# Kernel optimization log

Hardware: AMD Instinct MI355X
Metric: run time of the kernel (lower is better)

Reference implementation:

```python
import jax, jax.numpy as jnp
import numpy as np
from jax import lax

D_MODEL = 1024
D_STATE = 16
D_CONV = 4
EXPAND = 2
D_INNER = D_MODEL * EXPAND
EPS = 1e-6


def setup_inputs() -> dict:
    key = jax.random.key(0)
    ks = jax.random.split(key, 8)
    B, L = 2, 1024
    x = jax.random.normal(ks[0], (B, L, D_MODEL), dtype=jnp.float32)
    norm_w = jnp.ones((D_MODEL,), jnp.float32)
    W_in = jax.random.normal(ks[1], (2 * D_INNER, D_MODEL), jnp.float32) * (1.0 / np.sqrt(D_MODEL))
    conv_w = jax.random.normal(ks[2], (D_INNER, 1, D_CONV), jnp.float32) * (1.0 / np.sqrt(D_CONV))
    conv_b = jnp.zeros((D_INNER,), jnp.float32)
    W_x = jax.random.normal(ks[3], (2 * D_STATE + 1, D_INNER), jnp.float32) * (1.0 / np.sqrt(D_INNER))
    A_log = jnp.log(jnp.broadcast_to(jnp.arange(1, D_STATE + 1, dtype=jnp.float32), (D_INNER, D_STATE)))
    D_skip = jnp.ones((D_INNER,), jnp.float32)
    W_dt = jax.random.normal(ks[4], (D_INNER, 1), jnp.float32)
    b_dt = jax.random.normal(ks[5], (D_INNER,), jnp.float32) * 0.1
    W_out = jax.random.normal(ks[6], (D_MODEL, D_INNER), jnp.float32) * (1.0 / np.sqrt(D_INNER))
    return {"x": x, "norm_w": norm_w, "W_in": W_in, "conv_w": conv_w, "conv_b": conv_b,
            "W_x": W_x, "A_log": A_log, "D_skip": D_skip, "W_dt": W_dt, "b_dt": b_dt, "W_out": W_out}


def _selective_scan(x, delta, A, Bp, Cp, D_skip):
    # x, delta: (B, L, D); A: (D, N); Bp, Cp: (B, L, N)
    Bb, L, Dd = x.shape
    N = A.shape[1]

    def step(h, t_in):
        delta_t, B_t, C_t, x_t = t_in           # (B,D),(B,N),(B,N),(B,D)
        dA = jnp.exp(delta_t[..., None] * A)    # (B,D,N)
        h = dA * h + (delta_t * x_t)[..., None] * B_t[:, None, :]
        y_t = jnp.einsum('bdn,bn->bd', h, C_t)
        return h, y_t

    xs = (jnp.moveaxis(delta, 1, 0), jnp.moveaxis(Bp, 1, 0),
          jnp.moveaxis(Cp, 1, 0), jnp.moveaxis(x, 1, 0))
    h0 = jnp.zeros((Bb, Dd, N), x.dtype)
    _, ys = lax.scan(step, h0, xs)              # ys: (L,B,D)
    return jnp.moveaxis(ys, 0, 1) + x * D_skip


def reference(x, norm_w, W_in, conv_w, conv_b, W_x, A_log, D_skip, W_dt, b_dt, W_out):
    residual = x
    # RMSNorm
    xn = x * lax.rsqrt(jnp.mean(x * x, axis=-1, keepdims=True) + EPS) * norm_w
    # in_proj and split
    xz = xn @ W_in.T                              # (B,L,2*Din)
    x_ssm, z = jnp.split(xz, 2, axis=-1)
    # causal depthwise conv1d
    xc = jnp.swapaxes(x_ssm, 1, 2)                # (B,Din,L)
    xc = lax.conv_general_dilated(xc, conv_w, window_strides=(1,),
                                  padding=[(D_CONV - 1, 0)],
                                  feature_group_count=D_INNER,
                                  dimension_numbers=('NCH', 'OIH', 'NCH'))
    xc = xc + conv_b[None, :, None]
    x_ssm = jax.nn.silu(jnp.swapaxes(xc, 1, 2))   # (B,L,Din)
    # input-dependent SSM params
    ssm_params = x_ssm @ W_x.T                    # (B,L,2N+1)
    B_param = ssm_params[:, :, :D_STATE]
    C_param = ssm_params[:, :, D_STATE:2 * D_STATE]
    dt_raw = ssm_params[:, :, -1:]                # (B,L,1)
    delta = jax.nn.softplus(dt_raw * W_dt[:, 0] + b_dt)  # (B,L,Din)
    A = -jnp.exp(A_log)
    y = _selective_scan(x_ssm, delta, A, B_param, C_param, D_skip)
    y = y * jax.nn.silu(z)
    y = y @ W_out.T
    return y + residual
```

## Files before the change

kernel.cpp:

```cpp
#include <hip/hip_runtime.h>
#include <math.h>

#define D_MODEL 1024
#define D_STATE 16
#define D_CONV  4
#define D_INNER 2048
#define LSEQ    1024
#define BATCH   2
#define NROWS   (BATCH * LSEQ)
#define EPSV    1e-6f

#define CHUNK   64
#define NCHUNK  (LSEQ / CHUNK)
#define SSTATE  (BATCH * D_INNER * D_STATE)
#define SROW    36

typedef __attribute__((ext_vector_type(8))) short bf16x8;
typedef __attribute__((ext_vector_type(4))) float f32x4;

__device__ __forceinline__ float silu_f(float x) { return x / (1.0f + __expf(-x)); }
__device__ __forceinline__ float softplus_f(float x) {
    return (x > 20.0f) ? x : __logf(1.0f + __expf(x));
}
__device__ __forceinline__ unsigned short f2bf(float f) {
    unsigned int u = __float_as_uint(f);
    unsigned int r = (u + 0x7FFFu + ((u >> 16) & 1u)) >> 16;
    return (unsigned short)r;
}

__global__ __launch_bounds__(256) void cvt_bf16_kernel(const float* __restrict__ src,
                                                       unsigned short* __restrict__ dst) {
    int i = blockIdx.x * 256 + threadIdx.x;
    float4 v = ((const float4*)src)[i];
    ushort4 o;
    o.x = f2bf(v.x); o.y = f2bf(v.y); o.z = f2bf(v.z); o.w = f2bf(v.w);
    ((ushort4*)dst)[i] = o;
}

__global__ __launch_bounds__(256) void rmsnorm_kernel(const float* __restrict__ x,
                                                      const float* __restrict__ w,
                                                      unsigned short* __restrict__ xnb) {
    int row = blockIdx.x;
    const float4* xr = (const float4*)(x + (size_t)row * D_MODEL);
    float4 v = xr[threadIdx.x];
    float s = v.x * v.x + v.y * v.y + v.z * v.z + v.w * v.w;
#pragma unroll
    for (int off = 32; off > 0; off >>= 1) s += __shfl_down(s, off, 64);
    __shared__ float wsum[4];
    int lane = threadIdx.x & 63, wv = threadIdx.x >> 6;
    if (lane == 0) wsum[wv] = s;
    __syncthreads();
    float tot = wsum[0] + wsum[1] + wsum[2] + wsum[3];
    float scale = rsqrtf(tot * (1.0f / D_MODEL) + EPSV);
    const float4* wr = (const float4*)w;
    float4 wv4 = wr[threadIdx.x];
    ushort4 o;
    o.x = f2bf(v.x * scale * wv4.x);
    o.y = f2bf(v.y * scale * wv4.y);
    o.z = f2bf(v.z * scale * wv4.z);
    o.w = f2bf(v.w * scale * wv4.w);
    ((ushort4*)(xnb + (size_t)row * D_MODEL))[threadIdx.x] = o;
}

template<int TM, int TN, int JL>
__global__ __launch_bounds__(256) void gemm_bt_db(const short* __restrict__ A,
                                                  const short* __restrict__ B,
                                                  float* __restrict__ C,
                                                  const float* __restrict__ resid,
                                                  int M, int N, int K) {
    constexpr int MI = TM / 32, NJ = TN / 32;
    __shared__ alignas(16) short As[2][TM * 32];
    __shared__ alignas(16) short Bs[2][TN * 32];
    int tid = threadIdx.x;
    int wave = tid >> 6, lane = tid & 63;
    int wm = (wave >> 1) * (TM / 2), wn = (wave & 1) * (TN / 2);
    int m0 = blockIdx.y * TM, n0 = blockIdx.x * TN;

    f32x4 acc[MI][NJ];
#pragma unroll
    for (int i = 0; i < MI; i++)
#pragma unroll
        for (int j = 0; j < NJ; j++) acc[i][j] = (f32x4){0.f, 0.f, 0.f, 0.f};

    const short* Ab = A + (size_t)m0 * K;
    const short* Bb = B + (size_t)n0 * K;
    int qk = (lane >> 4) * 8;
    int rr = lane & 15;

    auto stage = [&](int k0, int buf) {
#pragma unroll
        for (int c0 = 0; c0 < TM * 4; c0 += 256) {
            int c = c0 + tid;
            __builtin_amdgcn_global_load_lds(
                (const __attribute__((address_space(1))) void*)(Ab + (size_t)(c >> 2) * K + k0 + (c & 3) * 8),
                (__attribute__((address_space(3))) void*)(&As[buf][c * 8]), 16, 0, 0);
        }
#pragma unroll
        for (int c0 = 0; c0 < TN * 4; c0 += 256) {
            int c = c0 + tid;
            __builtin_amdgcn_global_load_lds(
                (const __attribute__((address_space(1))) void*)(Bb + (size_t)(c >> 2) * K + k0 + (c & 3) * 8),
                (__attribute__((address_space(3))) void*)(&Bs[buf][c * 8]), 16, 0, 0);
        }
    };

    stage(0, 0);
    int KI = K / 32;
    for (int ki = 0; ki < KI; ki++) {
        int b = ki & 1;
        if (ki + 1 < KI) {
            stage((ki + 1) * 32, b ^ 1);
            __builtin_amdgcn_s_waitcnt(0xF70 | JL);
        } else {
            __builtin_amdgcn_s_waitcnt(0xF70);
        }
        __builtin_amdgcn_s_barrier();

        bf16x8 af[MI], bfr[NJ];
#pragma unroll
        for (int i = 0; i < MI; i++)
            af[i] = *(const bf16x8*)(&As[b][(wm + i * 16 + rr) * 32 + qk]);
#pragma unroll
        for (int j = 0; j < NJ; j++)
            bfr[j] = *(const bf16x8*)(&Bs[b][(wn + j * 16 + rr) * 32 + qk]);
#pragma unroll
        for (int i = 0; i < MI; i++)
#pragma unroll
            for (int j = 0; j < NJ; j++)
                acc[i][j] = __builtin_amdgcn_mfma_f32_16x16x32_bf16(af[i], bfr[j], acc[i][j], 0, 0, 0);
        __builtin_amdgcn_s_barrier();
    }

    int q4 = (lane >> 4) * 4;
#pragma unroll
    for (int i = 0; i < MI; i++) {
#pragma unroll
        for (int j = 0; j < NJ; j++) {
            int n = n0 + wn + j * 16 + rr;
#pragma unroll
            for (int v = 0; v < 4; v++) {
                int mm = m0 + wm + i * 16 + q4 + v;
                float val = acc[i][j][v];
                if (resid) val += resid[(size_t)mm * N + n];
                C[(size_t)mm * N + n] = val;
            }
        }
    }
}

__global__ __launch_bounds__(256) void conv_silu_kernel(const float* __restrict__ xz,
                                                        const float* __restrict__ w,
                                                        const float* __restrict__ cb,
                                                        float* __restrict__ xc) {
    int idx = blockIdx.x * 256 + threadIdx.x;
    int d = idx & (D_INNER - 1);
    int bl = idx >> 11;
    int l = bl & (LSEQ - 1);
    int bb = bl >> 10;
    float w0 = w[d * 4 + 0], w1 = w[d * 4 + 1], w2 = w[d * 4 + 2], w3 = w[d * 4 + 3];
    const float* base = xz + (size_t)(bb * LSEQ) * (2 * D_INNER) + d;
    float acc = cb[d];
    if (l >= 3) acc += w0 * base[(size_t)(l - 3) * (2 * D_INNER)];
    if (l >= 2) acc += w1 * base[(size_t)(l - 2) * (2 * D_INNER)];
    if (l >= 1) acc += w2 * base[(size_t)(l - 1) * (2 * D_INNER)];
    acc += w3 * base[(size_t)l * (2 * D_INNER)];
    xc[idx] = silu_f(acc);
}

#define PR 4
__global__ __launch_bounds__(256) void params_kernel(const float* __restrict__ xc,
                                                     const float* __restrict__ Wx,
                                                     float* __restrict__ ssm) {
    int r0 = blockIdx.x * PR;
    __shared__ alignas(16) float xs[PR][D_INNER];
    const float4* src = (const float4*)(xc + (size_t)r0 * D_INNER);
    for (int i = threadIdx.x; i < PR * D_INNER / 4; i += 256)
        ((float4*)xs)[i] = src[i];
    __syncthreads();
    int lane = threadIdx.x & 63, wv = threadIdx.x >> 6;
    for (int n = wv; n < 2 * D_STATE + 1; n += 4) {
        const float4* wrow = (const float4*)(Wx + (size_t)n * D_INNER);
        float s0 = 0.f, s1 = 0.f, s2 = 0.f, s3 = 0.f;
#pragma unroll
        for (int c = 0; c < D_INNER / 4 / 64; c++) {
            int k = c * 64 + lane;
            float4 w  = wrow[k];
            float4 a0 = *(const float4*)&xs[0][k * 4];
            float4 a1 = *(const float4*)&xs[1][k * 4];
            float4 a2 = *(const float4*)&xs[2][k * 4];
            float4 a3 = *(const float4*)&xs[3][k * 4];
            s0 += a0.x * w.x + a0.y * w.y + a0.z * w.z + a0.w * w.w;
            s1 += a1.x * w.x + a1.y * w.y + a1.z * w.z + a1.w * w.w;
            s2 += a2.x * w.x + a2.y * w.y + a2.z * w.z + a2.w * w.w;
            s3 += a3.x * w.x + a3.y * w.y + a3.z * w.z + a3.w * w.w;
        }
#pragma unroll
        for (int off = 32; off > 0; off >>= 1) {
            s0 += __shfl_down(s0, off, 64);
            s1 += __shfl_down(s1, off, 64);
            s2 += __shfl_down(s2, off, 64);
            s3 += __shfl_down(s3, off, 64);
        }
        if (lane == 0) {
            ssm[(size_t)(r0 + 0) * 33 + n] = s0;
            ssm[(size_t)(r0 + 1) * 33 + n] = s1;
            ssm[(size_t)(r0 + 2) * 33 + n] = s2;
            ssm[(size_t)(r0 + 3) * 33 + n] = s3;
        }
    }
}

__device__ __forceinline__ void stage_ssm(const float* __restrict__ ssm,
                                          float* __restrict__ s_ssm,
                                          int bb, int c, int tid) {
    int t = tid >> 2, j = tid & 3;
    const float* g = ssm + (size_t)(bb * LSEQ + c * CHUNK + t) * 33;
    float* s = s_ssm + t * SROW;
    for (int col = j; col < 33; col += 4) s[col] = g[col];
}

__global__ __launch_bounds__(256) void scanA_kernel(const float* __restrict__ ssm,
                                                    const float* __restrict__ xc,
                                                    const float* __restrict__ A_log,
                                                    const float* __restrict__ Wdt,
                                                    const float* __restrict__ bdt,
                                                    float* __restrict__ P,
                                                    float* __restrict__ Q) {
    int c = blockIdx.x, dg = blockIdx.y, bb = blockIdx.z;
    int tid = threadIdx.x;
    int d = dg * 256 + tid;
    __shared__ alignas(16) float s_ssm[CHUNK * SROW];
    stage_ssm(ssm, s_ssm, bb, c, tid);
    __syncthreads();

    float wdt = Wdt[d], bdtv = bdt[d];
    float Adn[16];
    {
        const float4* ar = (const float4*)(A_log + (size_t)d * 16);
#pragma unroll
        for (int r = 0; r < 4; r++) {
            float4 a = ar[r];
            Adn[r * 4 + 0] = -__expf(a.x);
            Adn[r * 4 + 1] = -__expf(a.y);
            Adn[r * 4 + 2] = -__expf(a.z);
            Adn[r * 4 + 3] = -__expf(a.w);
        }
    }
    float h[16];
#pragma unroll
    for (int n = 0; n < 16; n++) h[n] = 0.f;
    float sd = 0.f;
    const float* xg = xc + ((size_t)(bb * LSEQ + c * CHUNK)) * D_INNER + d;

#pragma unroll 2
    for (int t = 0; t < CHUNK; t++) {
        float dtr = s_ssm[t * SROW + 32];
        float dlt = softplus_f(dtr * wdt + bdtv);
        float xt = xg[(size_t)t * D_INNER];
        float u = dlt * xt;
        sd += dlt;
        const float4* Bq = (const float4*)&s_ssm[t * SROW];
#pragma unroll
        for (int r = 0; r < 4; r++) {
            float4 Bv = Bq[r];
            float dA0 = __expf(dlt * Adn[r * 4 + 0]);
            float dA1 = __expf(dlt * Adn[r * 4 + 1]);
            float dA2 = __expf(dlt * Adn[r * 4 + 2]);
            float dA3 = __expf(dlt * Adn[r * 4 + 3]);
            h[r * 4 + 0] = dA0 * h[r * 4 + 0] + u * Bv.x;
            h[r * 4 + 1] = dA1 * h[r * 4 + 1] + u * Bv.y;
            h[r * 4 + 2] = dA2 * h[r * 4 + 2] + u * Bv.z;
            h[r * 4 + 3] = dA3 * h[r * 4 + 3] + u * Bv.w;
        }
    }
    size_t idx = (size_t)c * SSTATE + ((size_t)bb * D_INNER + d) * 16;
#pragma unroll
    for (int r = 0; r < 4; r++) {
        float4 pv, qv;
        pv.x = __expf(Adn[r * 4 + 0] * sd);
        pv.y = __expf(Adn[r * 4 + 1] * sd);
        pv.z = __expf(Adn[r * 4 + 2] * sd);
        pv.w = __expf(Adn[r * 4 + 3] * sd);
        qv.x = h[r * 4 + 0]; qv.y = h[r * 4 + 1];
        qv.z = h[r * 4 + 2]; qv.w = h[r * 4 + 3];
        *(float4*)(P + idx + r * 4) = pv;
        *(float4*)(Q + idx + r * 4) = qv;
    }
}

__global__ __launch_bounds__(256) void scanB_kernel(float* __restrict__ P,
                                                    const float* __restrict__ Q) {
    int bdn = blockIdx.x * 256 + threadIdx.x;
    float H = 0.0f;
#pragma unroll
    for (int c = 0; c < NCHUNK; c++) {
        size_t idx = (size_t)c * SSTATE + bdn;
        float p = P[idx], q = Q[idx];
        P[idx] = H;
        H = p * H + q;
    }
}

__global__ __launch_bounds__(256) void scanC_kernel(const float* __restrict__ ssm,
                                                    const float* __restrict__ xc,
                                                    const float* __restrict__ xz,
                                                    const float* __restrict__ A_log,
                                                    const float* __restrict__ Wdt,
                                                    const float* __restrict__ bdt,
                                                    const float* __restrict__ Hs,
                                                    const float* __restrict__ Dskip,
                                                    unsigned short* __restrict__ yb) {
    int c = blockIdx.x, dg = blockIdx.y, bb = blockIdx.z;
    int tid = threadIdx.x;
    int d = dg * 256 + tid;
    __shared__ alignas(16) float s_ssm[CHUNK * SROW];
    stage_ssm(ssm, s_ssm, bb, c, tid);
    __syncthreads();

    float wdt = Wdt[d], bdtv = bdt[d], dsk = Dskip[d];
    float Adn[16];
    {
        const float4* ar = (const float4*)(A_log + (size_t)d * 16);
#pragma unroll
        for (int r = 0; r < 4; r++) {
            float4 a = ar[r];
            Adn[r * 4 + 0] = -__expf(a.x);
            Adn[r * 4 + 1] = -__expf(a.y);
            Adn[r * 4 + 2] = -__expf(a.z);
            Adn[r * 4 + 3] = -__expf(a.w);
        }
    }
    float h[16];
    {
        size_t idx = (size_t)c * SSTATE + ((size_t)bb * D_INNER + d) * 16;
#pragma unroll
        for (int r = 0; r < 4; r++) {
            float4 hv = *(const float4*)(Hs + idx + r * 4);
            h[r * 4 + 0] = hv.x; h[r * 4 + 1] = hv.y;
            h[r * 4 + 2] = hv.z; h[r * 4 + 3] = hv.w;
        }
    }
    const float* xg = xc + ((size_t)(bb * LSEQ + c * CHUNK)) * D_INNER + d;
    const float* zg = xz + ((size_t)(bb * LSEQ + c * CHUNK)) * (2 * D_INNER) + D_INNER + d;
    unsigned short* yg = yb + ((size_t)(bb * LSEQ + c * CHUNK)) * D_INNER + d;

#pragma unroll 2
    for (int t = 0; t < CHUNK; t++) {
        float dtr = s_ssm[t * SROW + 32];
        float dlt = softplus_f(dtr * wdt + bdtv);
        float xt = xg[(size_t)t * D_INNER];
        float zt = zg[(size_t)t * (2 * D_INNER)];
        float u = dlt * xt;
        const float4* Bq = (const float4*)&s_ssm[t * SROW];
        const float4* Cq = (const float4*)&s_ssm[t * SROW + 16];
        float y = 0.f;
#pragma unroll
        for (int r = 0; r < 4; r++) {
            float4 Bv = Bq[r];
            float4 Cv = Cq[r];
            float dA0 = __expf(dlt * Adn[r * 4 + 0]);
            float dA1 = __expf(dlt * Adn[r * 4 + 1]);
            float dA2 = __expf(dlt * Adn[r * 4 + 2]);
            float dA3 = __expf(dlt * Adn[r * 4 + 3]);
            h[r * 4 + 0] = dA0 * h[r * 4 + 0] + u * Bv.x;
            h[r * 4 + 1] = dA1 * h[r * 4 + 1] + u * Bv.y;
            h[r * 4 + 2] = dA2 * h[r * 4 + 2] + u * Bv.z;
            h[r * 4 + 3] = dA3 * h[r * 4 + 3] + u * Bv.w;
            y += h[r * 4 + 0] * Cv.x + h[r * 4 + 1] * Cv.y
               + h[r * 4 + 2] * Cv.z + h[r * 4 + 3] * Cv.w;
        }
        float o = (y + xt * dsk) * silu_f(zt);
        yg[(size_t)t * D_INNER] = f2bf(o);
    }
}

extern "C" void kernel_launch(void* const* d_in, const int* in_sizes, int n_in,
                              void* d_out, int out_size, void* d_ws, size_t ws_size,
                              hipStream_t stream) {
    const float* x      = (const float*)d_in[0];
    const float* norm_w = (const float*)d_in[1];
    const float* W_in   = (const float*)d_in[2];
    const float* conv_w = (const float*)d_in[3];
    const float* conv_b = (const float*)d_in[4];
    const float* W_x    = (const float*)d_in[5];
    const float* A_log  = (const float*)d_in[6];
    const float* D_skip = (const float*)d_in[7];
    const float* W_dt   = (const float*)d_in[8];
    const float* b_dt   = (const float*)d_in[9];
    const float* W_out  = (const float*)d_in[10];
    float* out = (float*)d_out;

    float* ws = (float*)d_ws;
    float* xz      = ws;
    float* xconv   = xz + (size_t)NROWS * 2 * D_INNER;
    float* ssm     = xconv + (size_t)NROWS * D_INNER;
    float* after   = ssm + (size_t)NROWS * 33;
    unsigned short* xnb    = (unsigned short*)after;
    unsigned short* W_in_b = (unsigned short*)(after + 1024 * 1024);
    unsigned short* W_out_b= (unsigned short*)(after + 3 * 1024 * 1024);
    unsigned short* ybuf_b = (unsigned short*)(after + 4 * 1024 * 1024);
    float* Pbuf = after + 1024 * 1024;
    float* Qbuf = Pbuf + (size_t)NCHUNK * SSTATE;

    cvt_bf16_kernel<<<(2 * D_INNER * D_MODEL) / 1024, 256, 0, stream>>>(W_in, W_in_b);
    cvt_bf16_kernel<<<(D_MODEL * D_INNER) / 1024, 256, 0, stream>>>(W_out, W_out_b);
    rmsnorm_kernel<<<NROWS, 256, 0, stream>>>(x, norm_w, xnb);
    {
        dim3 grid(2 * D_INNER / 128, NROWS / 64);
        gemm_bt_db<64, 128, 3><<<grid, 256, 0, stream>>>(
            (const short*)xnb, (const short*)W_in_b, xz, nullptr,
            NROWS, 2 * D_INNER, D_MODEL);
    }
    conv_silu_kernel<<<(NROWS * D_INNER) / 256, 256, 0, stream>>>(xz, conv_w, conv_b, xconv);
    params_kernel<<<NROWS / PR, 256, 0, stream>>>(xconv, W_x, ssm);
    {
        dim3 grid(NCHUNK, D_INNER / 256, BATCH);
        scanA_kernel<<<grid, 256, 0, stream>>>(ssm, xconv, A_log, W_dt, b_dt, Pbuf, Qbuf);
        scanB_kernel<<<SSTATE / 256, 256, 0, stream>>>(Pbuf, Qbuf);
        scanC_kernel<<<grid, 256, 0, stream>>>(ssm, xconv, xz, A_log, W_dt, b_dt,
                                               Pbuf, D_skip, ybuf_b);
    }
    {
        dim3 grid(D_MODEL / 64, NROWS / 64);
        gemm_bt_db<64, 64, 2><<<grid, 256, 0, stream>>>(
            (const short*)ybuf_b, (const short*)W_out_b, out, x,
            NROWS, D_MODEL, D_INNER);
    }
}
```

Measured before the change: 251.2 us.

## Split SSM state across 4 threads per channel in chunked scan kernels

The chunked scan kernels now give each channel to four threads, each holding four of the sixteen state entries, and reduce the C-projection with cross-lane shuffles. The grid grows fourfold along the channel axis. This shortens each thread's serial dependency chain and register footprint and raises the number of waves. In exchange, softplus, the x and z loads and the staging of shared memory are repeated across four times as many threads and blocks, and output stores are issued by only a quarter of the lanes.

```diff
diff --git a/kernel.cpp b/kernel.cpp
--- a/kernel.cpp
+++ b/kernel.cpp
@@ -210,6 +210,7 @@
     }
 }
 
+
 __device__ __forceinline__ void stage_ssm(const float* __restrict__ ssm,
                                           float* __restrict__ s_ssm,
                                           int bb, int c, int tid) {
@@ -228,64 +229,43 @@
                                                     float* __restrict__ Q) {
     int c = blockIdx.x, dg = blockIdx.y, bb = blockIdx.z;
     int tid = threadIdx.x;
-    int d = dg * 256 + tid;
+    int ch = tid >> 2, sg = tid & 3;
+    int d = dg * 64 + ch;
     __shared__ alignas(16) float s_ssm[CHUNK * SROW];
     stage_ssm(ssm, s_ssm, bb, c, tid);
     __syncthreads();
 
     float wdt = Wdt[d], bdtv = bdt[d];
-    float Adn[16];
-    {
-        const float4* ar = (const float4*)(A_log + (size_t)d * 16);
-#pragma unroll
-        for (int r = 0; r < 4; r++) {
-            float4 a = ar[r];
-            Adn[r * 4 + 0] = -__expf(a.x);
-            Adn[r * 4 + 1] = -__expf(a.y);
-            Adn[r * 4 + 2] = -__expf(a.z);
-            Adn[r * 4 + 3] = -__expf(a.w);
-        }
-    }
-    float h[16];
-#pragma unroll
-    for (int n = 0; n < 16; n++) h[n] = 0.f;
+    float Adn[4];
+    {
+        float4 a = *(const float4*)(A_log + (size_t)d * 16 + sg * 4);
+        Adn[0] = -__expf(a.x); Adn[1] = -__expf(a.y);
+        Adn[2] = -__expf(a.z); Adn[3] = -__expf(a.w);
+    }
+    float h[4] = {0.f, 0.f, 0.f, 0.f};
     float sd = 0.f;
     const float* xg = xc + ((size_t)(bb * LSEQ + c * CHUNK)) * D_INNER + d;
 
-#pragma unroll 2
+#pragma unroll 4
     for (int t = 0; t < CHUNK; t++) {
         float dtr = s_ssm[t * SROW + 32];
         float dlt = softplus_f(dtr * wdt + bdtv);
         float xt = xg[(size_t)t * D_INNER];
         float u = dlt * xt;
         sd += dlt;
-        const float4* Bq = (const float4*)&s_ssm[t * SROW];
-#pragma unroll
-        for (int r = 0; r < 4; r++) {
-            float4 Bv = Bq[r];
-            float dA0 = __expf(dlt * Adn[r * 4 + 0]);
-            float dA1 = __expf(dlt * Adn[r * 4 + 1]);
-            float dA2 = __expf(dlt * Adn[r * 4 + 2]);
-            float dA3 = __expf(dlt * Adn[r * 4 + 3]);
-            h[r * 4 + 0] = dA0 * h[r * 4 + 0] + u * Bv.x;
-            h[r * 4 + 1] = dA1 * h[r * 4 + 1] + u * Bv.y;
-            h[r * 4 + 2] = dA2 * h[r * 4 + 2] + u * Bv.z;
-            h[r * 4 + 3] = dA3 * h[r * 4 + 3] + u * Bv.w;
-        }
-    }
-    size_t idx = (size_t)c * SSTATE + ((size_t)bb * D_INNER + d) * 16;
-#pragma unroll
-    for (int r = 0; r < 4; r++) {
-        float4 pv, qv;
-        pv.x = __expf(Adn[r * 4 + 0] * sd);
-        pv.y = __expf(Adn[r * 4 + 1] * sd);
-        pv.z = __expf(Adn[r * 4 + 2] * sd);
-        pv.w = __expf(Adn[r * 4 + 3] * sd);
-        qv.x = h[r * 4 + 0]; qv.y = h[r * 4 + 1];
-        qv.z = h[r * 4 + 2]; qv.w = h[r * 4 + 3];
-        *(float4*)(P + idx + r * 4) = pv;
-        *(float4*)(Q + idx + r * 4) = qv;
-    }
+        float4 Bv = *(const float4*)&s_ssm[t * SROW + sg * 4];
+        h[0] = __expf(dlt * Adn[0]) * h[0] + u * Bv.x;
+        h[1] = __expf(dlt * Adn[1]) * h[1] + u * Bv.y;
+        h[2] = __expf(dlt * Adn[2]) * h[2] + u * Bv.z;
+        h[3] = __expf(dlt * Adn[3]) * h[3] + u * Bv.w;
+    }
+    size_t idx = (size_t)c * SSTATE + ((size_t)bb * D_INNER + d) * 16 + sg * 4;
+    float4 pv, qv;
+    pv.x = __expf(Adn[0] * sd); pv.y = __expf(Adn[1] * sd);
+    pv.z = __expf(Adn[2] * sd); pv.w = __expf(Adn[3] * sd);
+    qv.x = h[0]; qv.y = h[1]; qv.z = h[2]; qv.w = h[3];
+    *(float4*)(P + idx) = pv;
+    *(float4*)(Q + idx) = qv;
 }
 
 __global__ __launch_bounds__(256) void scanB_kernel(float* __restrict__ P,
@@ -312,65 +292,49 @@
                                                     unsigned short* __restrict__ yb) {
     int c = blockIdx.x, dg = blockIdx.y, bb = blockIdx.z;
     int tid = threadIdx.x;
-    int d = dg * 256 + tid;
+    int ch = tid >> 2, sg = tid & 3;
+    int d = dg * 64 + ch;
     __shared__ alignas(16) float s_ssm[CHUNK * SROW];
     stage_ssm(ssm, s_ssm, bb, c, tid);
     __syncthreads();
 
     float wdt = Wdt[d], bdtv = bdt[d], dsk = Dskip[d];
-    float Adn[16];
-    {
-        const float4* ar = (const float4*)(A_log + (size_t)d * 16);
-#pragma unroll
-        for (int r = 0; r < 4; r++) {
-            float4 a = ar[r];
-            Adn[r * 4 + 0] = -__expf(a.x);
-            Adn[r * 4 + 1] = -__expf(a.y);
-            Adn[r * 4 + 2] = -__expf(a.z);
-            Adn[r * 4 + 3] = -__expf(a.w);
-        }
-    }
-    float h[16];
-    {
-        size_t idx = (size_t)c * SSTATE + ((size_t)bb * D_INNER + d) * 16;
-#pragma unroll
-        for (int r = 0; r < 4; r++) {
-            float4 hv = *(const float4*)(Hs + idx + r * 4);
-            h[r * 4 + 0] = hv.x; h[r * 4 + 1] = hv.y;
-            h[r * 4 + 2] = hv.z; h[r * 4 + 3] = hv.w;
-        }
+    float Adn[4];
+    {
+        float4 a = *(const float4*)(A_log + (size_t)d * 16 + sg * 4);
+        Adn[0] = -__expf(a.x); Adn[1] = -__expf(a.y);
+        Adn[2] = -__expf(a.z); Adn[3] = -__expf(a.w);
+    }
+    float h[4];
+    {
+        float4 hv = *(const float4*)(Hs + (size_t)c * SSTATE
+                                     + ((size_t)bb * D_INNER + d) * 16 + sg * 4);
+        h[0] = hv.x; h[1] = hv.y; h[2] = hv.z; h[3] = hv.w;
     }
     const float* xg = xc + ((size_t)(bb * LSEQ + c * CHUNK)) * D_INNER + d;
     const float* zg = xz + ((size_t)(bb * LSEQ + c * CHUNK)) * (2 * D_INNER) + D_INNER + d;
     unsigned short* yg = yb + ((size_t)(bb * LSEQ + c * CHUNK)) * D_INNER + d;
 
-#pragma unroll 2
+#pragma unroll 4
     for (int t = 0; t < CHUNK; t++) {
         float dtr = s_ssm[t * SROW + 32];
         float dlt = softplus_f(dtr * wdt + bdtv);
         float xt = xg[(size_t)t * D_INNER];
         float zt = zg[(size_t)t * (2 * D_INNER)];
         float u = dlt * xt;
-        const float4* Bq = (const float4*)&s_ssm[t * SROW];
-        const float4* Cq = (const float4*)&s_ssm[t * SROW + 16];
-        float y = 0.f;
-#pragma unroll
-        for (int r = 0; r < 4; r++) {
-            float4 Bv = Bq[r];
-            float4 Cv = Cq[r];
-            float dA0 = __expf(dlt * Adn[r * 4 + 0]);
-            float dA1 = __expf(dlt * Adn[r * 4 + 1]);
-            float dA2 = __expf(dlt * Adn[r * 4 + 2]);
-            float dA3 = __expf(dlt * Adn[r * 4 + 3]);
-            h[r * 4 + 0] = dA0 * h[r * 4 + 0] + u * Bv.x;
-            h[r * 4 + 1] = dA1 * h[r * 4 + 1] + u * Bv.y;
-            h[r * 4 + 2] = dA2 * h[r * 4 + 2] + u * Bv.z;
-            h[r * 4 + 3] = dA3 * h[r * 4 + 3] + u * Bv.w;
-            y += h[r * 4 + 0] * Cv.x + h[r * 4 + 1] * Cv.y
-               + h[r * 4 + 2] * Cv.z + h[r * 4 + 3] * Cv.w;
-        }
-        float o = (y + xt * dsk) * silu_f(zt);
-        yg[(size_t)t * D_INNER] = f2bf(o);
+        float4 Bv = *(const float4*)&s_ssm[t * SROW + sg * 4];
+        float4 Cv = *(const float4*)&s_ssm[t * SROW + 16 + sg * 4];
+        h[0] = __expf(dlt * Adn[0]) * h[0] + u * Bv.x;
+        h[1] = __expf(dlt * Adn[1]) * h[1] + u * Bv.y;
+        h[2] = __expf(dlt * Adn[2]) * h[2] + u * Bv.z;
+        h[3] = __expf(dlt * Adn[3]) * h[3] + u * Bv.w;
+        float p = h[0] * Cv.x + h[1] * Cv.y + h[2] * Cv.z + h[3] * Cv.w;
+        p += __shfl_xor(p, 1, 64);
+        p += __shfl_xor(p, 2, 64);
+        if (sg == 0) {
+            float o = (p + xt * dsk) * silu_f(zt);
+            yg[(size_t)t * D_INNER] = f2bf(o);
+        }
     }
 }
 
@@ -414,7 +378,7 @@
     conv_silu_kernel<<<(NROWS * D_INNER) / 256, 256, 0, stream>>>(xz, conv_w, conv_b, xconv);
     params_kernel<<<NROWS / PR, 256, 0, stream>>>(xconv, W_x, ssm);
     {
-        dim3 grid(NCHUNK, D_INNER / 256, BATCH);
+        dim3 grid(NCHUNK, D_INNER / 64, BATCH);
         scanA_kernel<<<grid, 256, 0, stream>>>(ssm, xconv, A_log, W_dt, b_dt, Pbuf, Qbuf);
         scanB_kernel<<<SSTATE / 256, 256, 0, stream>>>(Pbuf, Qbuf);
         scanC_kernel<<<grid, 256, 0, stream>>>(ssm, xconv, xz, A_log, W_dt, b_dt,
```

Result: slower. 266.4 us (+6.0%).
